# Performance work log

Hardware: AMD Instinct MI355X
Metric: run time of the kernel (lower is better)

Reference implementation:

```python
import jax, jax.numpy as jnp
import numpy as np

B, T, C = 8, 2048, 256
H = 4
HD = C // H  # 64

def setup_inputs() -> dict:
    key = jax.random.key(0)
    ks = jax.random.split(key, 5)
    s = 1.0 / np.sqrt(C)
    return {
        "x": jax.random.normal(ks[0], (B, T, C), dtype=jnp.float32),
        "w_qkv": jax.random.uniform(ks[1], (3 * C, C), jnp.float32, -s, s),
        "b_qkv": jax.random.uniform(ks[2], (3 * C,), jnp.float32, -s, s),
        "w_proj": jax.random.uniform(ks[3], (C, C), jnp.float32, -s, s),
        "b_proj": jax.random.uniform(ks[4], (C,), jnp.float32, -s, s),
    }

def reference(x, w_qkv, b_qkv, w_proj, b_proj):
    # qkv projection: [B,T,3C] -> [3,B,H,T,HD]
    qkv = x @ w_qkv.T + b_qkv
    qkv = qkv.reshape(B, T, 3, H, HD).transpose(2, 0, 3, 1, 4)
    q, k, v = qkv[0], qkv[1], qkv[2]
    scale = HD ** -0.5
    attn = jnp.einsum("bhqd,bhkd->bhqk", q, k) * scale
    attn = jax.nn.softmax(attn, axis=-1)  # dropout is identity in eval
    out = jnp.einsum("bhqk,bhkd->bhqd", attn, v)
    out = out.transpose(0, 2, 1, 3).reshape(B, T, C)
    return out @ w_proj.T + b_proj
```

## Files before the change

### kernel.cpp

```cpp
#include <hip/hip_runtime.h>
#include <hip/hip_bf16.h>
#include <cstdint>
#include <cstddef>


typedef __attribute__((ext_vector_type(8))) __bf16 bf16x8;
typedef __attribute__((ext_vector_type(4))) float f32x4;
typedef __attribute__((ext_vector_type(16))) float f32x16;

__device__ __forceinline__ f32x4 mfma16(bf16x8 a, bf16x8 b, f32x4 c) {
  return __builtin_amdgcn_mfma_f32_16x16x32_bf16(a, b, c, 0, 0, 0);
}
__device__ __forceinline__ f32x16 mfma32(bf16x8 a, bf16x8 b, f32x16 c) {
  return __builtin_amdgcn_mfma_f32_32x32x16_bf16(a, b, c, 0, 0, 0);
}

__device__ __forceinline__ void gload_lds16(const void* g, void* l) {
  __builtin_amdgcn_global_load_lds(
      (const __attribute__((address_space(1))) void*)g,
      (__attribute__((address_space(3))) void*)l, 16, 0, 0);
}

__device__ __forceinline__ uint32_t cvtpk_bf16(float lo, float hi) {
  uint32_t r;
  asm("v_cvt_pk_bf16_f32 %0, %1, %2" : "=v"(r) : "v"(lo), "v"(hi));
  return r;
}

__global__ __launch_bounds__(256) void cast_all(
    const float* __restrict__ x, const float* __restrict__ wq,
    const float* __restrict__ wp,
    __bf16* __restrict__ xb, __bf16* __restrict__ wqb, __bf16* __restrict__ wpb) {
  const int NX = (16384 * 256) / 4, NQ = (768 * 256) / 4, NP = (256 * 256) / 4;
  int i = blockIdx.x * 256 + threadIdx.x;
  const float4* src;
  __bf16* dst;
  int j;
  if (i < NX) { src = (const float4*)x; dst = xb; j = i; }
  else if (i < NX + NQ) { src = (const float4*)wq; dst = wqb; j = i - NX; }
  else if (i < NX + NQ + NP) { src = (const float4*)wp; dst = wpb; j = i - NX - NQ; }
  else return;
  float4 v = src[j];
  union { __bf16 b[4]; ushort4 u; } o;
  o.b[0] = (__bf16)v.x; o.b[1] = (__bf16)v.y; o.b[2] = (__bf16)v.z; o.b[3] = (__bf16)v.w;
  ((ushort4*)dst)[j] = o.u;
}

template <int EPI>
__global__ __launch_bounds__(256) void gemm_nt(
    const __bf16* __restrict__ A, const __bf16* __restrict__ B,
    const float* __restrict__ bias, int K, int N,
    __bf16* __restrict__ qo, __bf16* __restrict__ ko, __bf16* __restrict__ vo,
    float* __restrict__ fo) {
  const int tid = threadIdx.x;
  const int lane = tid & 63;
  const int w = tid >> 6;
  const int wr = w >> 1, wc = w & 1;
  const int m0 = blockIdx.x * 128, n0 = blockIdx.y * 128;
  const int l15 = lane & 15, lhi = lane >> 4;
  const bool vswap = (EPI == 0) && (n0 >= 512);

  __shared__ __align__(16) __bf16 As[128 * 64];
  __shared__ __align__(16) __bf16 Bs[128 * 64];

  const f32x4 fzero = {0.f, 0.f, 0.f, 0.f};
  f32x4 acc[4][4];
#pragma unroll
  for (int i = 0; i < 4; i++)
#pragma unroll
    for (int j = 0; j < 4; j++) acc[i][j] = fzero;

  for (int k0 = 0; k0 < K; k0 += 64) {
#pragma unroll
    for (int it = 0; it < 4; ++it) {
      int c = it * 256 + tid;
      int row = c >> 3, cc = c & 7;
      int col = ((cc ^ (row & 7)) << 3);
      gload_lds16(A + (size_t)(m0 + row) * K + k0 + col, As + c * 8);
      gload_lds16(B + (size_t)(n0 + row) * K + k0 + col, Bs + c * 8);
    }
    asm volatile("s_waitcnt vmcnt(0)" ::: "memory");
    __syncthreads();

    bf16x8 af[4][2], bfr[4][2];
#pragma unroll
    for (int i = 0; i < 4; i++)
#pragma unroll
      for (int kk = 0; kk < 2; kk++) {
        af[i][kk]  = *(const bf16x8*)(
            As + (wr * 64 + i * 16 + l15) * 64 + (((kk * 4 + lhi) ^ (l15 & 7)) << 3));
        bfr[i][kk] = *(const bf16x8*)(
            Bs + (wc * 64 + i * 16 + l15) * 64 + (((kk * 4 + lhi) ^ (l15 & 7)) << 3));
      }
    __builtin_amdgcn_s_setprio(1);
    if (!vswap) {
#pragma unroll
      for (int kk = 0; kk < 2; kk++)
#pragma unroll
        for (int mi = 0; mi < 4; mi++)
#pragma unroll
          for (int ni = 0; ni < 4; ni++)
            acc[mi][ni] = mfma16(af[mi][kk], bfr[ni][kk], acc[mi][ni]);
    } else {
#pragma unroll
      for (int kk = 0; kk < 2; kk++)
#pragma unroll
        for (int mi = 0; mi < 4; mi++)
#pragma unroll
          for (int ni = 0; ni < 4; ni++)
            acc[mi][ni] = mfma16(bfr[ni][kk], af[mi][kk], acc[mi][ni]);
    }
    __builtin_amdgcn_s_setprio(0);
    __syncthreads();
  }

  if (vswap) {
#pragma unroll
    for (int mi = 0; mi < 4; mi++) {
#pragma unroll
      for (int ni = 0; ni < 4; ni++) {
        int tg = m0 + wr * 64 + mi * 16 + l15;
        int nb = n0 + wc * 64 + ni * 16 + (lhi << 2);
        int b = tg >> 11, t = tg & 2047;
#pragma unroll
        for (int r = 0; r < 4; r++) {
          int n = nb + r;
          float val = acc[mi][ni][r] + bias[n];
          int hd = n - 512;
          int h = hd >> 6, d = hd & 63;
          vo[((size_t)(b * 4 + h) * 64 + d) * 2048 + t] = (__bf16)val;
        }
      }
    }
    return;
  }

#pragma unroll
  for (int mi = 0; mi < 4; mi++) {
#pragma unroll
    for (int ni = 0; ni < 4; ni++) {
      int col = n0 + wc * 64 + ni * 16 + l15;
      int rowb = m0 + wr * 64 + mi * 16 + (lhi << 2);
      float bv = bias[col];
#pragma unroll
      for (int r = 0; r < 4; r++) {
        float val = acc[mi][ni][r] + bv;
        int rr = rowb + r;
        if (EPI == 0) {
          int h = (col >> 6) & 3;
          int d = col & 63;
          int b = rr >> 11;
          int t = rr & 2047;
          size_t bh = (size_t)(b * 4 + h);
          if (col < 256) {
            qo[(bh * 2048 + t) * 64 + d] = (__bf16)(val * 0.18033688f);
          } else {
            ko[(bh * 2048 + t) * 64 + d] = (__bf16)val;
          }
        } else {
          fo[(size_t)rr * N + col] = val;
        }
      }
    }
  }
}

__global__ __launch_bounds__(256, 2) void attn_kernel(
    const __bf16* __restrict__ Q, const __bf16* __restrict__ Kb,
    const __bf16* __restrict__ Vt, __bf16* __restrict__ Ao) {
  const int tid = threadIdx.x, lane = tid & 63, w = tid >> 6;
  const int l31 = lane & 31, hi = lane >> 5;
  const int bh = blockIdx.x;
  const int q0 = blockIdx.y * 128;
  const int b = bh >> 2, h = bh & 3;

  __shared__ __align__(16) __bf16 Ks[2][128 * 64];
  __shared__ __align__(16) __bf16 Vs[2][64 * 128];

  const __bf16* Qb = Q + (size_t)bh * 2048 * 64;
  const __bf16* Kbase = Kb + (size_t)bh * 2048 * 64;
  const __bf16* Vbase = Vt + (size_t)bh * 64 * 2048;

  const int qrow = q0 + w * 32 + l31;
  bf16x8 qf[4];
#pragma unroll
  for (int dc = 0; dc < 4; dc++)
    qf[dc] = *(const bf16x8*)(Qb + (size_t)qrow * 64 + dc * 16 + hi * 8);

  union { uint16_t u[8]; bf16x8 v; } onesu;
#pragma unroll
  for (int i = 0; i < 8; i++) onesu.u[i] = 0x3F80;
  const bf16x8 onef = onesu.v;

  f32x16 oacc[2], lacc;
#pragma unroll
  for (int i = 0; i < 16; i++) { oacc[0][i] = 0.f; oacc[1][i] = 0.f; lacc[i] = 0.f; }

  int kr[4], kc[4], vr[4], vc[4];
#pragma unroll
  for (int t = 0; t < 4; ++t) {
    int c = t * 256 + tid;
    kr[t] = c >> 3;
    kc[t] = (((c & 7) ^ (kr[t] & 7)) << 3);
    vr[t] = c >> 4;
    vc[t] = ((((c & 15) & 8) | (((c & 15) & 7) ^ (vr[t] & 7))) << 3);
  }

  {
#pragma unroll
    for (int t = 0; t < 4; ++t) {
      int c = t * 256 + tid;
      gload_lds16(Kbase + (size_t)kr[t] * 64 + kc[t], &Ks[0][c * 8]);
      gload_lds16(Vbase + (size_t)vr[t] * 2048 + vc[t], &Vs[0][c * 8]);
    }
  }

  int cur = 0;
  const int swz = (l31 & 7);

  for (int kt = 0; kt < 16; ++kt) {
    __syncthreads();

    if (kt + 1 < 16) {
      const __bf16* Kg = Kbase + (size_t)(kt + 1) * 128 * 64;
      const __bf16* Vg = Vbase + (size_t)(kt + 1) * 128;
#pragma unroll
      for (int t = 0; t < 4; ++t) {
        int c = t * 256 + tid;
        gload_lds16(Kg + (size_t)kr[t] * 64 + kc[t], &Ks[cur ^ 1][c * 8]);
        gload_lds16(Vg + (size_t)vr[t] * 2048 + vc[t], &Vs[cur ^ 1][c * 8]);
      }
    }

#pragma unroll
    for (int hf = 0; hf < 2; ++hf) {
      const __bf16* Kl = &Ks[cur][hf * 64 * 64];
      const __bf16* Vl = &Vs[cur][hf * 64];

      f32x16 sacc[2];
#pragma unroll
      for (int i = 0; i < 16; i++) { sacc[0][i] = -16.f; sacc[1][i] = -16.f; }
#pragma unroll
      for (int kb = 0; kb < 2; kb++) {
        bf16x8 kf[4];
#pragma unroll
        for (int dc = 0; dc < 4; dc++)
          kf[dc] = *(const bf16x8*)(
              Kl + (kb * 32 + l31) * 64 + (((dc * 2 + hi) ^ swz) << 3));
        __builtin_amdgcn_s_setprio(1);
#pragma unroll
        for (int dc = 0; dc < 4; dc++)
          sacc[kb] = mfma32(kf[dc], qf[dc], sacc[kb]);
        __builtin_amdgcn_s_setprio(0);
      }

#pragma unroll
      for (int kb = 0; kb < 2; kb++)
#pragma unroll
        for (int i = 0; i < 16; i++) sacc[kb][i] = exp2f(sacc[kb][i]);

      uint32_t wo[8][2];
#pragma unroll
      for (int kb = 0; kb < 2; kb++)
#pragma unroll
        for (int e = 0; e < 4; e++) {
          wo[kb * 4 + e][0] = cvtpk_bf16(sacc[kb][4 * e + 0], sacc[kb][4 * e + 1]);
          wo[kb * 4 + e][1] = cvtpk_bf16(sacc[kb][4 * e + 2], sacc[kb][4 * e + 3]);
        }
      bf16x8 pa[4];
#pragma unroll
      for (int ks = 0; ks < 4; ks++) {
        uint32_t a0 = wo[2 * ks][0], b0 = wo[2 * ks + 1][0];
        uint32_t a1 = wo[2 * ks][1], b1 = wo[2 * ks + 1][1];
        asm("v_permlane32_swap_b32 %0, %1" : "+v"(a0), "+v"(b0));
        asm("v_permlane32_swap_b32 %0, %1" : "+v"(a1), "+v"(b1));
        union { uint32_t u[4]; bf16x8 v; } f;
        f.u[0] = a0; f.u[1] = a1; f.u[2] = b0; f.u[3] = b1;
        pa[ks] = f.v;
      }

#pragma unroll
      for (int db = 0; db < 2; db++) {
        bf16x8 vf[4];
#pragma unroll
        for (int ks = 0; ks < 4; ks++)
          vf[ks] = *(const bf16x8*)(
              Vl + (db * 32 + l31) * 128 + (((ks * 2 + hi) ^ swz) << 3));
        __builtin_amdgcn_s_setprio(1);
#pragma unroll
        for (int ks = 0; ks < 4; ks++)
          oacc[db] = mfma32(pa[ks], vf[ks], oacc[db]);
        __builtin_amdgcn_s_setprio(0);
      }
      __builtin_amdgcn_s_setprio(1);
#pragma unroll
      for (int ks = 0; ks < 4; ks++)
        lacc = mfma32(pa[ks], onef, lacc);
      __builtin_amdgcn_s_setprio(0);
    }

    cur ^= 1;
  }

#pragma unroll
  for (int db = 0; db < 2; db++)
#pragma unroll
    for (int r = 0; r < 16; r++) {
      int qr = 4 * hi + (r & 3) + 8 * (r >> 2);
      int t = q0 + w * 32 + qr;
      Ao[((size_t)(b * 2048 + t)) * 256 + h * 64 + db * 32 + l31] =
          (__bf16)(oacc[db][r] / lacc[r]);
    }
}

extern "C" void kernel_launch(void* const* d_in, const int* in_sizes, int n_in,
                              void* d_out, int out_size, void* d_ws, size_t ws_size,
                              hipStream_t stream) {
  const float* x      = (const float*)d_in[0];
  const float* w_qkv  = (const float*)d_in[1];
  const float* b_qkv  = (const float*)d_in[2];
  const float* w_proj = (const float*)d_in[3];
  const float* b_proj = (const float*)d_in[4];
  float* out = (float*)d_out;

  char* ws = (char*)d_ws;
  __bf16* xb  = (__bf16*)ws; ws += (size_t)16384 * 256 * 2;
  __bf16* wqb = (__bf16*)ws; ws += (size_t)768 * 256 * 2;
  __bf16* wpb = (__bf16*)ws; ws += (size_t)256 * 256 * 2;
  __bf16* qb  = (__bf16*)ws; ws += (size_t)8 * 4 * 2048 * 64 * 2;
  __bf16* kb  = (__bf16*)ws; ws += (size_t)8 * 4 * 2048 * 64 * 2;
  __bf16* vb  = (__bf16*)ws; ws += (size_t)8 * 4 * 2048 * 64 * 2;
  __bf16* aob = (__bf16*)ws; ws += (size_t)16384 * 256 * 2;

  int castN = (16384 * 256 + 768 * 256 + 256 * 256) / 4;
  cast_all<<<(castN + 255) / 256, 256, 0, stream>>>(x, w_qkv, w_proj, xb, wqb, wpb);
  gemm_nt<0><<<dim3(128, 6), 256, 0, stream>>>(xb, wqb, b_qkv, 256, 768,
                                               qb, kb, vb, nullptr);
  attn_kernel<<<dim3(32, 16), 256, 0, stream>>>(qb, kb, vb, aob);
  gemm_nt<1><<<dim3(128, 2), 256, 0, stream>>>(aob, wpb, b_proj, 256, 256,
                                               nullptr, nullptr, nullptr, out);
}
```

Before: 158.5 us.

## Template GEMM N-tile width and batch QK^T for both halves before softmax

Adds a BN template parameter to the GEMM so the output projection runs with 64-wide N tiles over a 128x4 grid, doubling block count for better CU occupancy on a small GEMM. Separately, the attention loop now computes the QK^T scores for both 64-key halves before running exp and PV, which gives the scheduler more independent MFMA work to interleave. In exchange, the projection re-reads the A tile twice as often, and holding two sets of score accumulators raises register pressure in the attention kernel.

```diff
diff --git a/kernel.cpp b/kernel.cpp
--- a/kernel.cpp
+++ b/kernel.cpp
@@ -46,29 +46,30 @@
   ((ushort4*)dst)[j] = o.u;
 }
 
-template <int EPI>
+template <int EPI, int BN>
 __global__ __launch_bounds__(256) void gemm_nt(
     const __bf16* __restrict__ A, const __bf16* __restrict__ B,
     const float* __restrict__ bias, int K, int N,
     __bf16* __restrict__ qo, __bf16* __restrict__ ko, __bf16* __restrict__ vo,
     float* __restrict__ fo) {
+  constexpr int NI = BN / 32;
   const int tid = threadIdx.x;
   const int lane = tid & 63;
   const int w = tid >> 6;
   const int wr = w >> 1, wc = w & 1;
-  const int m0 = blockIdx.x * 128, n0 = blockIdx.y * 128;
+  const int m0 = blockIdx.x * 128, n0 = blockIdx.y * BN;
   const int l15 = lane & 15, lhi = lane >> 4;
   const bool vswap = (EPI == 0) && (n0 >= 512);
 
   __shared__ __align__(16) __bf16 As[128 * 64];
-  __shared__ __align__(16) __bf16 Bs[128 * 64];
+  __shared__ __align__(16) __bf16 Bs[BN * 64];
 
   const f32x4 fzero = {0.f, 0.f, 0.f, 0.f};
-  f32x4 acc[4][4];
+  f32x4 acc[4][NI];
 #pragma unroll
   for (int i = 0; i < 4; i++)
 #pragma unroll
-    for (int j = 0; j < 4; j++) acc[i][j] = fzero;
+    for (int j = 0; j < NI; j++) acc[i][j] = fzero;
 
   for (int k0 = 0; k0 < K; k0 += 64) {
 #pragma unroll
@@ -77,21 +78,30 @@
       int row = c >> 3, cc = c & 7;
       int col = ((cc ^ (row & 7)) << 3);
       gload_lds16(A + (size_t)(m0 + row) * K + k0 + col, As + c * 8);
+    }
+#pragma unroll
+    for (int it = 0; it < NI; ++it) {
+      int c = it * 256 + tid;
+      int row = c >> 3, cc = c & 7;
+      int col = ((cc ^ (row & 7)) << 3);
       gload_lds16(B + (size_t)(n0 + row) * K + k0 + col, Bs + c * 8);
     }
     asm volatile("s_waitcnt vmcnt(0)" ::: "memory");
     __syncthreads();
 
-    bf16x8 af[4][2], bfr[4][2];
+    bf16x8 af[4][2], bfr[NI][2];
 #pragma unroll
     for (int i = 0; i < 4; i++)
 #pragma unroll
-      for (int kk = 0; kk < 2; kk++) {
-        af[i][kk]  = *(const bf16x8*)(
+      for (int kk = 0; kk < 2; kk++)
+        af[i][kk] = *(const bf16x8*)(
             As + (wr * 64 + i * 16 + l15) * 64 + (((kk * 4 + lhi) ^ (l15 & 7)) << 3));
+#pragma unroll
+    for (int i = 0; i < NI; i++)
+#pragma unroll
+      for (int kk = 0; kk < 2; kk++)
         bfr[i][kk] = *(const bf16x8*)(
-            Bs + (wc * 64 + i * 16 + l15) * 64 + (((kk * 4 + lhi) ^ (l15 & 7)) << 3));
-      }
+            Bs + (wc * (BN / 2) + i * 16 + l15) * 64 + (((kk * 4 + lhi) ^ (l15 & 7)) << 3));
     __builtin_amdgcn_s_setprio(1);
     if (!vswap) {
 #pragma unroll
@@ -99,7 +109,7 @@
 #pragma unroll
         for (int mi = 0; mi < 4; mi++)
 #pragma unroll
-          for (int ni = 0; ni < 4; ni++)
+          for (int ni = 0; ni < NI; ni++)
             acc[mi][ni] = mfma16(af[mi][kk], bfr[ni][kk], acc[mi][ni]);
     } else {
 #pragma unroll
@@ -107,39 +117,41 @@
 #pragma unroll
         for (int mi = 0; mi < 4; mi++)
 #pragma unroll
-          for (int ni = 0; ni < 4; ni++)
+          for (int ni = 0; ni < NI; ni++)
             acc[mi][ni] = mfma16(bfr[ni][kk], af[mi][kk], acc[mi][ni]);
     }
     __builtin_amdgcn_s_setprio(0);
     __syncthreads();
   }
 
-  if (vswap) {
-#pragma unroll
-    for (int mi = 0; mi < 4; mi++) {
-#pragma unroll
-      for (int ni = 0; ni < 4; ni++) {
-        int tg = m0 + wr * 64 + mi * 16 + l15;
-        int nb = n0 + wc * 64 + ni * 16 + (lhi << 2);
-        int b = tg >> 11, t = tg & 2047;
-#pragma unroll
-        for (int r = 0; r < 4; r++) {
-          int n = nb + r;
-          float val = acc[mi][ni][r] + bias[n];
-          int hd = n - 512;
-          int h = hd >> 6, d = hd & 63;
-          vo[((size_t)(b * 4 + h) * 64 + d) * 2048 + t] = (__bf16)val;
+  if constexpr (EPI == 0) {
+    if (vswap) {
+#pragma unroll
+      for (int mi = 0; mi < 4; mi++) {
+#pragma unroll
+        for (int ni = 0; ni < NI; ni++) {
+          int tg = m0 + wr * 64 + mi * 16 + l15;
+          int nb = n0 + wc * (BN / 2) + ni * 16 + (lhi << 2);
+          int b = tg >> 11, t = tg & 2047;
+#pragma unroll
+          for (int r = 0; r < 4; r++) {
+            int n = nb + r;
+            float val = acc[mi][ni][r] + bias[n];
+            int hd = n - 512;
+            int h = hd >> 6, d = hd & 63;
+            vo[((size_t)(b * 4 + h) * 64 + d) * 2048 + t] = (__bf16)val;
+          }
         }
       }
-    }
-    return;
+      return;
+    }
   }
 
 #pragma unroll
   for (int mi = 0; mi < 4; mi++) {
 #pragma unroll
-    for (int ni = 0; ni < 4; ni++) {
-      int col = n0 + wc * 64 + ni * 16 + l15;
+    for (int ni = 0; ni < NI; ni++) {
+      int col = n0 + wc * (BN / 2) + ni * 16 + l15;
       int rowb = m0 + wr * 64 + mi * 16 + (lhi << 2);
       float bv = bias[col];
 #pragma unroll
@@ -232,14 +244,12 @@
       }
     }
 
+    f32x16 sacc[2][2];
 #pragma unroll
     for (int hf = 0; hf < 2; ++hf) {
       const __bf16* Kl = &Ks[cur][hf * 64 * 64];
-      const __bf16* Vl = &Vs[cur][hf * 64];
-
-      f32x16 sacc[2];
-#pragma unroll
-      for (int i = 0; i < 16; i++) { sacc[0][i] = -16.f; sacc[1][i] = -16.f; }
+#pragma unroll
+      for (int i = 0; i < 16; i++) { sacc[hf][0][i] = -16.f; sacc[hf][1][i] = -16.f; }
 #pragma unroll
       for (int kb = 0; kb < 2; kb++) {
         bf16x8 kf[4];
@@ -250,22 +260,27 @@
         __builtin_amdgcn_s_setprio(1);
 #pragma unroll
         for (int dc = 0; dc < 4; dc++)
-          sacc[kb] = mfma32(kf[dc], qf[dc], sacc[kb]);
+          sacc[hf][kb] = mfma32(kf[dc], qf[dc], sacc[hf][kb]);
         __builtin_amdgcn_s_setprio(0);
       }
+    }
+
+#pragma unroll
+    for (int hf = 0; hf < 2; ++hf) {
+      const __bf16* Vl = &Vs[cur][hf * 64];
 
 #pragma unroll
       for (int kb = 0; kb < 2; kb++)
 #pragma unroll
-        for (int i = 0; i < 16; i++) sacc[kb][i] = exp2f(sacc[kb][i]);
+        for (int i = 0; i < 16; i++) sacc[hf][kb][i] = exp2f(sacc[hf][kb][i]);
 
       uint32_t wo[8][2];
 #pragma unroll
       for (int kb = 0; kb < 2; kb++)
 #pragma unroll
         for (int e = 0; e < 4; e++) {
-          wo[kb * 4 + e][0] = cvtpk_bf16(sacc[kb][4 * e + 0], sacc[kb][4 * e + 1]);
-          wo[kb * 4 + e][1] = cvtpk_bf16(sacc[kb][4 * e + 2], sacc[kb][4 * e + 3]);
+          wo[kb * 4 + e][0] = cvtpk_bf16(sacc[hf][kb][4 * e + 0], sacc[hf][kb][4 * e + 1]);
+          wo[kb * 4 + e][1] = cvtpk_bf16(sacc[hf][kb][4 * e + 2], sacc[hf][kb][4 * e + 3]);
         }
       bf16x8 pa[4];
 #pragma unroll
@@ -334,9 +349,9 @@
 
   int castN = (16384 * 256 + 768 * 256 + 256 * 256) / 4;
   cast_all<<<(castN + 255) / 256, 256, 0, stream>>>(x, w_qkv, w_proj, xb, wqb, wpb);
-  gemm_nt<0><<<dim3(128, 6), 256, 0, stream>>>(xb, wqb, b_qkv, 256, 768,
-                                               qb, kb, vb, nullptr);
+  gemm_nt<0, 128><<<dim3(128, 6), 256, 0, stream>>>(xb, wqb, b_qkv, 256, 768,
+                                                    qb, kb, vb, nullptr);
   attn_kernel<<<dim3(32, 16), 256, 0, stream>>>(qb, kb, vb, aob);
-  gemm_nt<1><<<dim3(128, 2), 256, 0, stream>>>(aob, wpb, b_proj, 256, 256,
-                                               nullptr, nullptr, nullptr, out);
-}
+  gemm_nt<1, 64><<<dim3(128, 4), 256, 0, stream>>>(aob, wpb, b_proj, 256, 256,
+                                                   nullptr, nullptr, nullptr, out);
+}
```

Result: no change. 156.8 us (-1.1%).
